# Performance work log

Measured on AMD Instinct MI355X. Metric: run time of the kernel, lower is better.

Reference implementation:

```python
import jax, jax.numpy as jnp
import numpy as np

EMBED_DIM = 1024
NUM_HEADS = 16
HEAD_DIM = EMBED_DIM // NUM_HEADS
MAX_REL = 64
B, S = 4, 1024


def setup_inputs() -> dict:
    key = jax.random.key(0)
    ks = jax.random.split(key, 12)
    scale = 1.0 / np.sqrt(EMBED_DIM)
    inp = {
        "query": jax.random.normal(ks[0], (B, S, EMBED_DIM), jnp.float32),
        "key": jax.random.normal(ks[1], (B, S, EMBED_DIM), jnp.float32),
        "value": jax.random.normal(ks[2], (B, S, EMBED_DIM), jnp.float32),
        "attn_mask": jnp.ones((B, 1, S, S), jnp.int32),
        # projection weights stored [in, out] so x @ W matches torch Linear(x) with W = weight.T
        "Wq": jax.random.normal(ks[3], (EMBED_DIM, EMBED_DIM), jnp.float32) * scale,
        "bq": jnp.zeros((EMBED_DIM,), jnp.float32),
        "Wk": jax.random.normal(ks[4], (EMBED_DIM, EMBED_DIM), jnp.float32) * scale,
        "bk": jnp.zeros((EMBED_DIM,), jnp.float32),
        "Wv": jax.random.normal(ks[5], (EMBED_DIM, EMBED_DIM), jnp.float32) * scale,
        "bv": jnp.zeros((EMBED_DIM,), jnp.float32),
        "Wo": jax.random.normal(ks[6], (EMBED_DIM, EMBED_DIM), jnp.float32) * scale,
        "bo": jnp.zeros((EMBED_DIM,), jnp.float32),
        "rel_pos_embed": jax.random.normal(ks[7], (2 * MAX_REL + 1, HEAD_DIM), jnp.float32) * 0.02,
    }
    return inp


def _split_heads(x):
    # [B, S, E] -> [B, H, S, D]
    b, s, _ = x.shape
    return x.reshape(b, s, NUM_HEADS, HEAD_DIM).transpose(0, 2, 1, 3)


def reference(query, key, value, attn_mask, Wq, bq, Wk, bk, Wv, bv, Wo, bo, rel_pos_embed):
    q = _split_heads(query @ Wq + bq)
    k = _split_heads(key @ Wk + bk)
    v = _split_heads(value @ Wv + bv)

    scores = jnp.einsum("bhqd,bhkd->bhqk", q, k) / np.sqrt(HEAD_DIM).astype(np.float32)

    # relative position bias: rel_pos[i, j] = rel_pos_embed[clip(i - j) + MAX_REL]
    seq_len = scores.shape[-1]
    rng = jnp.arange(seq_len)
    range_mat = jnp.clip(rng[:, None] - rng[None, :], -MAX_REL, MAX_REL) + MAX_REL
    rel_pos = rel_pos_embed[range_mat]                       # [S, S, D]
    # torch: matmul(q[...,None,:], rel_pos.mT).squeeze(-2) == einsum over head_dim (NOT scaled)
    rel_scores = jnp.einsum("bhid,ijd->bhij", q, rel_pos)
    scores = scores + rel_scores

    scores = jnp.where(attn_mask == 0, -jnp.inf, scores)
    attn_weights = jax.nn.softmax(scores, axis=-1)           # dropout p=0.0 -> identity

    out = jnp.einsum("bhqk,bhkd->bhqd", attn_weights, v)
    out = out.transpose(0, 2, 1, 3).reshape(query.shape[0], -1, EMBED_DIM)
    out = out @ Wo + bo
    return out, attn_weights
```

## Files before the change

### kernel.cpp

```cpp
#include <hip/hip_runtime.h>
#include <math.h>

#define BB 4
#define SS 1024
#define EE 1024
#define HH 16
#define DD 64
#define RR 129
#define PRELW 130

typedef __attribute__((ext_vector_type(4))) float f32x4;
typedef __attribute__((ext_vector_type(4))) int   i32x4;
typedef __attribute__((ext_vector_type(8))) short bf8;
typedef __attribute__((ext_vector_type(4))) short s4v;

#define MFMA(a, b, c) __builtin_amdgcn_mfma_f32_16x16x32_bf16(a, b, c, 0, 0, 0)

__device__ __forceinline__ float bf2f(unsigned short u) {
    return __uint_as_float(((unsigned)u) << 16);
}
__device__ __forceinline__ unsigned short f2bf(float x) {
    unsigned u = __float_as_uint(x);
    return (unsigned short)((u + 0x7fffu + ((u >> 16) & 1u)) >> 16);
}

__global__ __launch_bounds__(256, 4)
void wtrans_kernel(const float* __restrict__ Wq, const float* __restrict__ Wk,
                   const float* __restrict__ Wv, const float* __restrict__ Wo,
                   unsigned short* __restrict__ wt_hi, unsigned short* __restrict__ wt_lo)
{
    __shared__ float T[64][65];
    const int w = blockIdx.z;
    const float* W = w == 0 ? Wq : (w == 1 ? Wk : (w == 2 ? Wv : Wo));
    const int n0 = blockIdx.x * 64, k0 = blockIdx.y * 64;
    const int tid = threadIdx.x;
#pragma unroll
    for (int i = 0; i < 4; ++i) {
        int c = tid + 256 * i; int r = c >> 4, c4 = c & 15;
        f32x4 v = *(const f32x4*)(W + (size_t)(k0 + r) * EE + n0 + c4 * 4);
        T[r][c4 * 4 + 0] = v.x; T[r][c4 * 4 + 1] = v.y;
        T[r][c4 * 4 + 2] = v.z; T[r][c4 * 4 + 3] = v.w;
    }
    __syncthreads();
#pragma unroll
    for (int i = 0; i < 4; ++i) {
        int c = tid + 256 * i; int r = c >> 4, c4 = c & 15;
        float x0 = T[c4 * 4 + 0][r], x1 = T[c4 * 4 + 1][r];
        float x2 = T[c4 * 4 + 2][r], x3 = T[c4 * 4 + 3][r];
        unsigned short h0 = f2bf(x0), h1 = f2bf(x1), h2 = f2bf(x2), h3 = f2bf(x3);
        unsigned short l0 = f2bf(x0 - bf2f(h0)), l1 = f2bf(x1 - bf2f(h1));
        unsigned short l2 = f2bf(x2 - bf2f(h2)), l3 = f2bf(x3 - bf2f(h3));
        size_t o = (size_t)w * 1048576 + (size_t)(n0 + r) * 1024 + k0 + c4 * 4;
        *(s4v*)&wt_hi[o] = (s4v){(short)h0, (short)h1, (short)h2, (short)h3};
        *(s4v*)&wt_lo[o] = (s4v){(short)l0, (short)l1, (short)l2, (short)l3};
    }
}

__global__ __launch_bounds__(256)
void maskbits_kernel(const int* __restrict__ mask, unsigned long long* __restrict__ mb)
{
    const int w = blockIdx.x * 256 + threadIdx.x;
    const int* p = mask + (size_t)w * 64;
    unsigned long long bits = 0;
#pragma unroll
    for (int i = 0; i < 16; ++i) {
        int4 v = *(const int4*)(p + i * 4);
        bits |= (unsigned long long)(v.x != 0) << (i * 4 + 0);
        bits |= (unsigned long long)(v.y != 0) << (i * 4 + 1);
        bits |= (unsigned long long)(v.z != 0) << (i * 4 + 2);
        bits |= (unsigned long long)(v.w != 0) << (i * 4 + 3);
    }
    mb[w] = bits;
}

template<int ASRC, int EPI>
__device__ __forceinline__ void gemm_body(
    const float* __restrict__ Af,
    const unsigned short* __restrict__ Ah_g, const unsigned short* __restrict__ Al_g,
    const unsigned short* __restrict__ Bh_g, const unsigned short* __restrict__ Bl_g,
    const float* __restrict__ bias,
    float* __restrict__ Yf, unsigned short* __restrict__ Yh, unsigned short* __restrict__ Yl,
    unsigned short* As_h, unsigned short* As_l, unsigned short* Bs_h, unsigned short* Bs_l,
    int m0, int n0)
{
    const int tid = threadIdx.x, lane = tid & 63, wid = tid >> 6;
    const int wm = (wid >> 1) * 64, wn = (wid & 1) * 64;
    f32x4 zero4 = {0.f, 0.f, 0.f, 0.f};
    f32x4 acc[4][4];
#pragma unroll
    for (int a = 0; a < 4; ++a)
#pragma unroll
        for (int b = 0; b < 4; ++b) acc[a][b] = zero4;

    for (int kt = 0; kt < 1024; kt += 64) {
        __syncthreads();
        if (ASRC == 0) {
#pragma unroll
            for (int i = 0; i < 8; ++i) {
                int c = tid + 256 * i; int r = c >> 4, c4 = c & 15;
                f32x4 v = *(const f32x4*)(Af + (size_t)(m0 + r) * 1024 + kt + c4 * 4);
                unsigned short h0 = f2bf(v.x), h1 = f2bf(v.y), h2 = f2bf(v.z), h3 = f2bf(v.w);
                unsigned short l0 = f2bf(v.x - bf2f(h0)), l1 = f2bf(v.y - bf2f(h1));
                unsigned short l2 = f2bf(v.z - bf2f(h2)), l3 = f2bf(v.w - bf2f(h3));
                int off = r * 64 + (((c4 >> 1) ^ (r & 7)) * 8) + (c4 & 1) * 4;
                *(s4v*)&As_h[off] = (s4v){(short)h0, (short)h1, (short)h2, (short)h3};
                *(s4v*)&As_l[off] = (s4v){(short)l0, (short)l1, (short)l2, (short)l3};
            }
        } else {
#pragma unroll
            for (int i = 0; i < 4; ++i) {
                int c = tid + 256 * i; int r = c >> 3, cc = c & 7;
                int off = r * 64 + ((cc ^ (r & 7)) * 8);
                *(bf8*)&As_h[off] = *(const bf8*)(Ah_g + (size_t)(m0 + r) * 1024 + kt + cc * 8);
                *(bf8*)&As_l[off] = *(const bf8*)(Al_g + (size_t)(m0 + r) * 1024 + kt + cc * 8);
            }
        }
#pragma unroll
        for (int i = 0; i < 4; ++i) {
            int c = tid + 256 * i; int r = c >> 3, cc = c & 7;
            int off = r * 64 + ((cc ^ (r & 7)) * 8);
            *(bf8*)&Bs_h[off] = *(const bf8*)(Bh_g + (size_t)(n0 + r) * 1024 + kt + cc * 8);
            *(bf8*)&Bs_l[off] = *(const bf8*)(Bl_g + (size_t)(n0 + r) * 1024 + kt + cc * 8);
        }
        __syncthreads();
#pragma unroll
        for (int ks = 0; ks < 2; ++ks) {
            bf8 ah[4], al[4], bh[4], bl[4];
#pragma unroll
            for (int f = 0; f < 4; ++f) {
                int ra = wm + f * 16 + (lane & 15);
                int ca = (ks * 4 + (lane >> 4)) ^ (ra & 7);
                ah[f] = *(const bf8*)&As_h[ra * 64 + ca * 8];
                al[f] = *(const bf8*)&As_l[ra * 64 + ca * 8];
                int rb = wn + f * 16 + (lane & 15);
                int cb = (ks * 4 + (lane >> 4)) ^ (rb & 7);
                bh[f] = *(const bf8*)&Bs_h[rb * 64 + cb * 8];
                bl[f] = *(const bf8*)&Bs_l[rb * 64 + cb * 8];
            }
#pragma unroll
            for (int fi = 0; fi < 4; ++fi)
#pragma unroll
                for (int fj = 0; fj < 4; ++fj) {
                    acc[fi][fj] = MFMA(ah[fi], bh[fj], acc[fi][fj]);
                    acc[fi][fj] = MFMA(al[fi], bh[fj], acc[fi][fj]);
                    acc[fi][fj] = MFMA(ah[fi], bl[fj], acc[fi][fj]);
                }
        }
    }
#pragma unroll
    for (int fi = 0; fi < 4; ++fi)
#pragma unroll
        for (int fj = 0; fj < 4; ++fj)
#pragma unroll
            for (int rg = 0; rg < 4; ++rg) {
                int m = m0 + wm + fi * 16 + ((lane >> 4) << 2) + rg;
                int n = n0 + wn + fj * 16 + (lane & 15);
                float val = acc[fi][fj][rg] + bias[n];
                if (EPI == 0) {
                    int b = m >> 10, s = m & 1023, h = n >> 6, d = n & 63;
                    size_t o = (((size_t)(b * 16 + h)) * 1024 + s) * 64 + d;
                    unsigned short hv = f2bf(val);
                    unsigned short lv = f2bf(val - bf2f(hv));
                    Yh[o] = hv; Yl[o] = lv;
                } else {
                    Yf[(size_t)m * 1024 + n] = val;
                }
            }
}

__global__ __launch_bounds__(256, 2)
void proj_qkv_kernel(const float* __restrict__ q_in, const float* __restrict__ k_in,
                     const float* __restrict__ v_in,
                     const unsigned short* __restrict__ wt_hi, const unsigned short* __restrict__ wt_lo,
                     const float* __restrict__ bq, const float* __restrict__ bk,
                     const float* __restrict__ bv,
                     unsigned short* qh_hi, unsigned short* qh_lo,
                     unsigned short* kh_hi, unsigned short* kh_lo,
                     unsigned short* vh_hi, unsigned short* vh_lo)
{
    __shared__ __align__(16) unsigned short As_h[128 * 64], As_l[128 * 64];
    __shared__ __align__(16) unsigned short Bs_h[128 * 64], Bs_l[128 * 64];
    const int z = blockIdx.z;
    const float* X = z == 0 ? q_in : (z == 1 ? k_in : v_in);
    const float* bias = z == 0 ? bq : (z == 1 ? bk : bv);
    unsigned short* Yh = z == 0 ? qh_hi : (z == 1 ? kh_hi : vh_hi);
    unsigned short* Yl = z == 0 ? qh_lo : (z == 1 ? kh_lo : vh_lo);
    gemm_body<0, 0>(X, nullptr, nullptr,
                    wt_hi + (size_t)z * 1048576, wt_lo + (size_t)z * 1048576,
                    bias, nullptr, Yh, Yl, As_h, As_l, Bs_h, Bs_l,
                    blockIdx.x * 128, blockIdx.y * 128);
}

__global__ __launch_bounds__(256, 2)
void outproj_kernel(const unsigned short* __restrict__ ctx_hi, const unsigned short* __restrict__ ctx_lo,
                    const unsigned short* __restrict__ wo_hi, const unsigned short* __restrict__ wo_lo,
                    const float* __restrict__ bo, float* __restrict__ out)
{
    __shared__ __align__(16) unsigned short As_h[128 * 64], As_l[128 * 64];
    __shared__ __align__(16) unsigned short Bs_h[128 * 64], Bs_l[128 * 64];
    gemm_body<1, 1>(nullptr, ctx_hi, ctx_lo, wo_hi, wo_lo, bo, out, nullptr, nullptr,
                    As_h, As_l, Bs_h, Bs_l, blockIdx.x * 128, blockIdx.y * 128);
}

__global__ __launch_bounds__(256, 4)
void vtrans_kernel(const unsigned short* __restrict__ vh_hi, const unsigned short* __restrict__ vh_lo,
                   unsigned short* __restrict__ vt_hi, unsigned short* __restrict__ vt_lo)
{
    __shared__ unsigned short T[64][72];
    const unsigned short* src = blockIdx.z ? vh_lo : vh_hi;
    unsigned short* dst = blockIdx.z ? vt_lo : vt_hi;
    const int st = blockIdx.x * 64, bh = blockIdx.y, tid = threadIdx.x;
#pragma unroll
    for (int i = 0; i < 4; ++i) {
        int c = tid + 256 * i; int r = c >> 4, d4 = c & 15;
        s4v v = *(const s4v*)(src + ((size_t)bh * 1024 + st + r) * 64 + d4 * 4);
        T[r][d4 * 4 + 0] = (unsigned short)v.x; T[r][d4 * 4 + 1] = (unsigned short)v.y;
        T[r][d4 * 4 + 2] = (unsigned short)v.z; T[r][d4 * 4 + 3] = (unsigned short)v.w;
    }
    __syncthreads();
#pragma unroll
    for (int i = 0; i < 4; ++i) {
        int c = tid + 256 * i; int r = c >> 4, s4_ = c & 15;
        s4v o = {(short)T[s4_ * 4 + 0][r], (short)T[s4_ * 4 + 1][r],
                 (short)T[s4_ * 4 + 2][r], (short)T[s4_ * 4 + 3][r]};
        *(s4v*)(dst + ((size_t)bh * 64 + r) * 1024 + st + s4_ * 4) = o;
    }
}

__global__ __launch_bounds__(256, 2)
void attn_fused_kernel(const unsigned short* __restrict__ qh_hi, const unsigned short* __restrict__ qh_lo,
                       const unsigned short* __restrict__ kh_hi, const unsigned short* __restrict__ kh_lo,
                       const unsigned short* __restrict__ vt_hi, const unsigned short* __restrict__ vt_lo,
                       const float* __restrict__ emb, const unsigned long long* __restrict__ mb,
                       float* __restrict__ attn,
                       unsigned short* __restrict__ ctx_hi, unsigned short* __restrict__ ctx_lo)
{
    __shared__ __align__(16) unsigned short Sh[128 * 64], Sl[128 * 64];
    __shared__ __align__(16) unsigned short Pr[128 * PRELW];
    __shared__ float Sm[2][128], Ss[2][128], SmF[128], SsF[128];
    const int tid = threadIdx.x, lane = tid & 63, wid = tid >> 6;
    const int wi = wid >> 1, wj = wid & 1;
    const int g = lane >> 4, li = lane & 15;
    const int bh = blockIdx.x, i0 = blockIdx.y * 128, b = bh >> 4;
    const f32x4 zero4 = {0.f, 0.f, 0.f, 0.f};

    const unsigned short* qbh = qh_hi + ((size_t)bh * 1024 + i0) * 64;
    const unsigned short* qbl = qh_lo + ((size_t)bh * 1024 + i0) * 64;
#pragma unroll
    for (int i = 0; i < 4; ++i) {
        int c = tid + 256 * i; int r = c >> 3, cc = c & 7;
        int off = r * 64 + ((cc ^ (r & 7)) * 8);
        *(bf8*)&Sh[off] = *(const bf8*)(qbh + r * 64 + cc * 8);
        *(bf8*)&Sl[off] = *(const bf8*)(qbl + r * 64 + cc * 8);
    }
    __syncthreads();

    bf8 qfh[4][2], qfl[4][2];
#pragma unroll
    for (int fi = 0; fi < 4; ++fi)
#pragma unroll
        for (int ks = 0; ks < 2; ++ks) {
            int rb = wi * 64 + fi * 16 + li;
            int cb = (ks * 4 + g) ^ (rb & 7);
            qfh[fi][ks] = *(const bf8*)&Sh[rb * 64 + cb * 8];
            qfl[fi][ks] = *(const bf8*)&Sl[rb * 64 + cb * 8];
        }

    for (int t = wid; t < 72; t += 4) {
        const int it = t / 9, rt = t % 9;
        f32x4 pc = zero4;
#pragma unroll
        for (int ks = 0; ks < 2; ++ks) {
            int ra = it * 16 + li;
            int ca = (ks * 4 + g) ^ (ra & 7);
            bf8 aq = *(const bf8*)&Sh[ra * 64 + ca * 8];
            int er = rt * 16 + li; if (er > 128) er = 128;
            const float* ep = emb + (size_t)er * 64 + ks * 32 + g * 8;
            f32x4 e0 = *(const f32x4*)ep;
            f32x4 e1 = *(const f32x4*)(ep + 4);
            bf8 be = {(short)f2bf(e0.x), (short)f2bf(e0.y), (short)f2bf(e0.z), (short)f2bf(e0.w),
                      (short)f2bf(e1.x), (short)f2bf(e1.y), (short)f2bf(e1.z), (short)f2bf(e1.w)};
            pc = MFMA(aq, be, pc);
        }
        const int rcol = rt * 16 + li;
        if (rcol < RR) {
#pragma unroll
            for (int rg = 0; rg < 4; ++rg)
                Pr[(it * 16 + g * 4 + rg) * PRELW + rcol] = f2bf(pc[rg]);
        }
    }

    float rm[4], rs[4];
#pragma unroll
    for (int i = 0; i < 4; ++i) { rm[i] = -3.0e38f; rs[i] = 0.f; }

    for (int jt = 0; jt < 8; ++jt) {
        __syncthreads();
        const unsigned short* kbh = kh_hi + ((size_t)bh * 1024 + jt * 128) * 64;
        const unsigned short* kbl = kh_lo + ((size_t)bh * 1024 + jt * 128) * 64;
#pragma unroll
        for (int i = 0; i < 4; ++i) {
            int c = tid + 256 * i; int r = c >> 3, cc = c & 7;
            int off = r * 64 + ((cc ^ (r & 7)) * 8);
            *(bf8*)&Sh[off] = *(const bf8*)(kbh + r * 64 + cc * 8);
            *(bf8*)&Sl[off] = *(const bf8*)(kbl + r * 64 + cc * 8);
        }
        __syncthreads();
        f32x4 acc[4][4];
#pragma unroll
        for (int a = 0; a < 4; ++a)
#pragma unroll
            for (int c = 0; c < 4; ++c) acc[a][c] = zero4;
#pragma unroll
        for (int ks = 0; ks < 2; ++ks) {
            bf8 kfh[4], kfl[4];
#pragma unroll
            for (int fj = 0; fj < 4; ++fj) {
                int ra = wj * 64 + fj * 16 + li;
                int ca = (ks * 4 + g) ^ (ra & 7);
                kfh[fj] = *(const bf8*)&Sh[ra * 64 + ca * 8];
                kfl[fj] = *(const bf8*)&Sl[ra * 64 + ca * 8];
            }
#pragma unroll
            for (int fj = 0; fj < 4; ++fj)
#pragma unroll
                for (int fi = 0; fi < 4; ++fi) {
                    acc[fj][fi] = MFMA(kfh[fj], qfh[fi][ks], acc[fj][fi]);
                    acc[fj][fi] = MFMA(kfl[fj], qfh[fi][ks], acc[fj][fi]);
                    acc[fj][fi] = MFMA(kfh[fj], qfl[fi][ks], acc[fj][fi]);
                }
        }
#pragma unroll
        for (int fi = 0; fi < 4; ++fi) {
            const int rowL = wi * 64 + fi * 16 + li;
            const int ii = i0 + rowL;
            const unsigned long long mw = mb[((size_t)b * 1024 + ii) * 16 + jt * 2 + wj];
            float p16[4][4];
            float tmax = -3.0e38f;
#pragma unroll
            for (int fj = 0; fj < 4; ++fj)
#pragma unroll
                for (int rg = 0; rg < 4; ++rg) {
                    int jloc = fj * 16 + g * 4 + rg;
                    int jj = jt * 128 + wj * 64 + jloc;
                    int dd = ii - jj; dd = dd < -64 ? -64 : (dd > 64 ? 64 : dd);
                    float s = acc[fj][fi][rg] * 0.125f + bf2f(Pr[rowL * PRELW + dd + 64]);
                    if (!((mw >> jloc) & 1ull)) s = -1.0e30f;
                    p16[fj][rg] = s;
                    tmax = fmaxf(tmax, s);
                }
            tmax = fmaxf(tmax, __shfl_xor(tmax, 16, 64));
            tmax = fmaxf(tmax, __shfl_xor(tmax, 32, 64));
            float nm = fmaxf(rm[fi], tmax);
            float ps = 0.f;
#pragma unroll
            for (int fj = 0; fj < 4; ++fj)
#pragma unroll
                for (int rg = 0; rg < 4; ++rg) ps += __expf(p16[fj][rg] - nm);
            ps += __shfl_xor(ps, 16, 64);
            ps += __shfl_xor(ps, 32, 64);
            rs[fi] = rs[fi] * __expf(rm[fi] - nm) + ps;
            rm[fi] = nm;
        }
    }
#pragma unroll
    for (int fi = 0; fi < 4; ++fi) {
        if (lane < 16) {
            Sm[wj][wi * 64 + fi * 16 + li] = rm[fi];
            Ss[wj][wi * 64 + fi * 16 + li] = rs[fi];
        }
    }
    __syncthreads();
    if (tid < 128) {
        float m0_ = Sm[0][tid], m1_ = Sm[1][tid];
        float mmx = fmaxf(m0_, m1_);
        SmF[tid] = mmx;
        SsF[tid] = Ss[0][tid] * __expf(m0_ - mmx) + Ss[1][tid] * __expf(m1_ - mmx);
    }
    __syncthreads();
    float mm4[4], iv4[4];
#pragma unroll
    for (int fi = 0; fi < 4; ++fi) {
        mm4[fi] = SmF[wi * 64 + fi * 16 + li];
        iv4[fi] = 1.f / SsF[wi * 64 + fi * 16 + li];
    }

    f32x4 ctx_acc[4][4];
#pragma unroll
    for (int a = 0; a < 4; ++a)
#pragma unroll
        for (int c = 0; c < 4; ++c) ctx_acc[a][c] = zero4;

    for (int jt = 0; jt < 8; ++jt) {
        __syncthreads();
        const unsigned short* kbh = kh_hi + ((size_t)bh * 1024 + jt * 128) * 64;
        const unsigned short* kbl = kh_lo + ((size_t)bh * 1024 + jt * 128) * 64;
#pragma unroll
        for (int i = 0; i < 4; ++i) {
            int c = tid + 256 * i; int r = c >> 3, cc = c & 7;
            int off = r * 64 + ((cc ^ (r & 7)) * 8);
            *(bf8*)&Sh[off] = *(const bf8*)(kbh + r * 64 + cc * 8);
            *(bf8*)&Sl[off] = *(const bf8*)(kbl + r * 64 + cc * 8);
        }
        __syncthreads();
        f32x4 acc[4][4];
#pragma unroll
        for (int a = 0; a < 4; ++a)
#pragma unroll
            for (int c = 0; c < 4; ++c) acc[a][c] = zero4;
#pragma unroll
        for (int ks = 0; ks < 2; ++ks) {
            bf8 kfh[4], kfl[4];
#pragma unroll
            for (int fj = 0; fj < 4; ++fj) {
                int ra = wj * 64 + fj * 16 + li;
                int ca = (ks * 4 + g) ^ (ra & 7);
                kfh[fj] = *(const bf8*)&Sh[ra * 64 + ca * 8];
                kfl[fj] = *(const bf8*)&Sl[ra * 64 + ca * 8];
            }
#pragma unroll
            for (int fj = 0; fj < 4; ++fj)
#pragma unroll
                for (int fi = 0; fi < 4; ++fi) {
                    acc[fj][fi] = MFMA(kfh[fj], qfh[fi][ks], acc[fj][fi]);
                    acc[fj][fi] = MFMA(kfl[fj], qfh[fi][ks], acc[fj][fi]);
                    acc[fj][fi] = MFMA(kfh[fj], qfl[fi][ks], acc[fj][fi]);
                }
        }
#pragma unroll
        for (int c = 0; c < 2; ++c) {
            bf8 vfh[4], vfl[4];
#pragma unroll
            for (int fd = 0; fd < 4; ++fd) {
                size_t vb = (size_t)bh * 65536 + (size_t)(fd * 16 + li) * 1024
                          + jt * 128 + wj * 64 + c * 32 + g * 8;
                vfh[fd] = *(const bf8*)(vt_hi + vb);
                vfl[fd] = *(const bf8*)(vt_lo + vb);
            }
#pragma unroll
            for (int fi = 0; fi < 4; ++fi) {
                const int rowL = wi * 64 + fi * 16 + li;
                const int ii = i0 + rowL;
                const unsigned long long mw = mb[((size_t)b * 1024 + ii) * 16 + jt * 2 + wj];
                const float mmf = mm4[fi], ivf = iv4[fi];
                float* arow = attn + ((size_t)bh * 1024 + ii) * 1024 + jt * 128 + wj * 64 + g * 4;
                unsigned wh[2][2], wl[2][2];
#pragma unroll
                for (int t = 0; t < 2; ++t) {
                    const int fj = c * 2 + t;
                    f32x4 pv;
#pragma unroll
                    for (int rg = 0; rg < 4; ++rg) {
                        int jloc = fj * 16 + g * 4 + rg;
                        int jj = jt * 128 + wj * 64 + jloc;
                        int dd = ii - jj; dd = dd < -64 ? -64 : (dd > 64 ? 64 : dd);
                        float s = acc[fj][fi][rg] * 0.125f + bf2f(Pr[rowL * PRELW + dd + 64]);
                        if (!((mw >> jloc) & 1ull)) s = -1.0e30f;
                        pv[rg] = __expf(s - mmf) * ivf;
                    }
                    *(f32x4*)(arow + fj * 16) = pv;
                    unsigned short h0 = f2bf(pv.x), h1 = f2bf(pv.y), h2 = f2bf(pv.z), h3 = f2bf(pv.w);
                    wh[t][0] = (unsigned)h0 | ((unsigned)h1 << 16);
                    wh[t][1] = (unsigned)h2 | ((unsigned)h3 << 16);
                    unsigned short l0 = f2bf(pv.x - bf2f(h0)), l1 = f2bf(pv.y - bf2f(h1));
                    unsigned short l2 = f2bf(pv.z - bf2f(h2)), l3 = f2bf(pv.w - bf2f(h3));
                    wl[t][0] = (unsigned)l0 | ((unsigned)l1 << 16);
                    wl[t][1] = (unsigned)l2 | ((unsigned)l3 << 16);
                }
                const int src0 = ((g & 1) * 2) * 16 + li;
                const int src1 = src0 + 16;
                const bool hiT = (g >> 1) & 1;
                int x0A = __shfl((int)wh[0][0], src0, 64), x0B = __shfl((int)wh[1][0], src0, 64);
                int x1A = __shfl((int)wh[0][1], src0, 64), x1B = __shfl((int)wh[1][1], src0, 64);
                int x2A = __shfl((int)wh[0][0], src1, 64), x2B = __shfl((int)wh[1][0], src1, 64);
                int x3A = __shfl((int)wh[0][1], src1, 64), x3B = __shfl((int)wh[1][1], src1, 64);
                i32x4 awh = {hiT ? x0B : x0A, hiT ? x1B : x1A, hiT ? x2B : x2A, hiT ? x3B : x3A};
                bf8 pah = *(bf8*)&awh;
                int y0A = __shfl((int)wl[0][0], src0, 64), y0B = __shfl((int)wl[1][0], src0, 64);
                int y1A = __shfl((int)wl[0][1], src0, 64), y1B = __shfl((int)wl[1][1], src0, 64);
                int y2A = __shfl((int)wl[0][0], src1, 64), y2B = __shfl((int)wl[1][0], src1, 64);
                int y3A = __shfl((int)wl[0][1], src1, 64), y3B = __shfl((int)wl[1][1], src1, 64);
                i32x4 awl = {hiT ? y0B : y0A, hiT ? y1B : y1A, hiT ? y2B : y2A, hiT ? y3B : y3A};
                bf8 pal = *(bf8*)&awl;
#pragma unroll
                for (int fd = 0; fd < 4; ++fd) {
                    ctx_acc[fi][fd] = MFMA(pah, vfh[fd], ctx_acc[fi][fd]);
                    ctx_acc[fi][fd] = MFMA(pal, vfh[fd], ctx_acc[fi][fd]);
                    ctx_acc[fi][fd] = MFMA(pah, vfl[fd], ctx_acc[fi][fd]);
                }
            }
        }
    }

    __syncthreads();
    float* red = (wi == 0) ? (float*)Sh : (float*)Sl;
    if (wj == 1) {
#pragma unroll
        for (int fi = 0; fi < 4; ++fi)
#pragma unroll
            for (int fd = 0; fd < 4; ++fd)
#pragma unroll
                for (int rg = 0; rg < 4; ++rg) {
                    int idx = (fi * 4 + fd) * 4 + rg;
                    red[lane * 64 + ((idx + lane) & 63)] = ctx_acc[fi][fd][rg];
                }
    }
    __syncthreads();
    if (wj == 0) {
        const int b_ = bh >> 4, h = bh & 15;
#pragma unroll
        for (int fi = 0; fi < 4; ++fi)
#pragma unroll
            for (int fd = 0; fd < 4; ++fd)
#pragma unroll
                for (int rg = 0; rg < 4; ++rg) {
                    int idx = (fi * 4 + fd) * 4 + rg;
                    float val = ctx_acc[fi][fd][rg] + red[lane * 64 + ((idx + lane) & 63)];
                    int ii = i0 + wi * 64 + fi * 16 + g * 4 + rg;
                    int d = fd * 16 + li;
                    size_t o = ((size_t)b_ * 1024 + ii) * 1024 + h * 64 + d;
                    unsigned short hv = f2bf(val);
                    unsigned short lv = f2bf(val - bf2f(hv));
                    ctx_hi[o] = hv;
                    ctx_lo[o] = lv;
                }
    }
}

extern "C" void kernel_launch(void* const* d_in, const int* in_sizes, int n_in,
                              void* d_out, int out_size, void* d_ws, size_t ws_size,
                              hipStream_t stream)
{
    const float* query = (const float*)d_in[0];
    const float* key_  = (const float*)d_in[1];
    const float* value = (const float*)d_in[2];
    const int*   mask  = (const int*)d_in[3];
    const float* Wq = (const float*)d_in[4];
    const float* bq = (const float*)d_in[5];
    const float* Wk = (const float*)d_in[6];
    const float* bk = (const float*)d_in[7];
    const float* Wv = (const float*)d_in[8];
    const float* bv = (const float*)d_in[9];
    const float* Wo = (const float*)d_in[10];
    const float* bo = (const float*)d_in[11];
    const float* emb = (const float*)d_in[12];

    unsigned short* wt_hi = (unsigned short*)d_ws;
    unsigned short* wt_lo = wt_hi + (size_t)4 * 1048576;
    unsigned short* qh_hi = wt_lo + (size_t)4 * 1048576;
    unsigned short* qh_lo = qh_hi + 4194304;
    unsigned short* kh_hi = qh_lo + 4194304;
    unsigned short* kh_lo = kh_hi + 4194304;
    unsigned short* vt_hi = kh_lo + 4194304;
    unsigned short* vt_lo = vt_hi + 4194304;
    unsigned short* ctx_hi = vt_lo + 4194304;
    unsigned short* ctx_lo = ctx_hi + 4194304;
    unsigned long long* mb = (unsigned long long*)d_ws;
    unsigned short* vh_hi = (unsigned short*)d_out;
    unsigned short* vh_lo = vh_hi + 4194304;

    float* out  = (float*)d_out;
    float* attn = (float*)d_out + 4194304;

    dim3 blk(256);
    wtrans_kernel<<<dim3(16, 16, 4), blk, 0, stream>>>(Wq, Wk, Wv, Wo, wt_hi, wt_lo);
    proj_qkv_kernel<<<dim3(32, 8, 3), blk, 0, stream>>>(query, key_, value, wt_hi, wt_lo,
                                                        bq, bk, bv, qh_hi, qh_lo,
                                                        kh_hi, kh_lo, vh_hi, vh_lo);
    maskbits_kernel<<<dim3(256), blk, 0, stream>>>(mask, mb);
    vtrans_kernel<<<dim3(16, 64, 2), blk, 0, stream>>>(vh_hi, vh_lo, vt_hi, vt_lo);
    attn_fused_kernel<<<dim3(64, 8), blk, 0, stream>>>(qh_hi, qh_lo, kh_hi, kh_lo,
                                                       vt_hi, vt_lo, emb, mb,
                                                       attn, ctx_hi, ctx_lo);
    outproj_kernel<<<dim3(32, 8), blk, 0, stream>>>(ctx_hi, ctx_lo,
                                                    wt_hi + (size_t)3 * 1048576,
                                                    wt_lo + (size_t)3 * 1048576, bo, out);
}
```

Before: 539.2 us.

## Halve K tile to 64 rows to cut LDS and registers for three blocks per CU

Shrinks the shared K/Q staging buffers from 128 to 64 rows, loads Q and builds the relative-position table in two 64-row halves, and iterates the key loop 16 times with 64-key tiles. This lowers per-thread accumulator registers and LDS usage so launch bounds can request three blocks per CU, aiming at more latency hiding. The final cross-wave reduction buffer moves into the Pr region, and attention-weight stores become nontemporal to avoid polluting cache. The cost is twice as many barriers and tile loads, and smaller MFMA batches per sync.

```diff
diff --git a/kernel.cpp b/kernel.cpp
--- a/kernel.cpp
+++ b/kernel.cpp
@@ -227,7 +227,7 @@
     }
 }
 
-__global__ __launch_bounds__(256, 2)
+__global__ __launch_bounds__(256, 3)
 void attn_fused_kernel(const unsigned short* __restrict__ qh_hi, const unsigned short* __restrict__ qh_lo,
                        const unsigned short* __restrict__ kh_hi, const unsigned short* __restrict__ kh_lo,
                        const unsigned short* __restrict__ vt_hi, const unsigned short* __restrict__ vt_lo,
@@ -235,7 +235,7 @@
                        float* __restrict__ attn,
                        unsigned short* __restrict__ ctx_hi, unsigned short* __restrict__ ctx_lo)
 {
-    __shared__ __align__(16) unsigned short Sh[128 * 64], Sl[128 * 64];
+    __shared__ __align__(16) unsigned short Sh[64 * 64], Sl[64 * 64];
     __shared__ __align__(16) unsigned short Pr[128 * PRELW];
     __shared__ float Sm[2][128], Ss[2][128], SmF[128], SsF[128];
     const int tid = threadIdx.x, lane = tid & 63, wid = tid >> 6;
@@ -246,83 +246,87 @@
 
     const unsigned short* qbh = qh_hi + ((size_t)bh * 1024 + i0) * 64;
     const unsigned short* qbl = qh_lo + ((size_t)bh * 1024 + i0) * 64;
-#pragma unroll
-    for (int i = 0; i < 4; ++i) {
-        int c = tid + 256 * i; int r = c >> 3, cc = c & 7;
-        int off = r * 64 + ((cc ^ (r & 7)) * 8);
-        *(bf8*)&Sh[off] = *(const bf8*)(qbh + r * 64 + cc * 8);
-        *(bf8*)&Sl[off] = *(const bf8*)(qbl + r * 64 + cc * 8);
-    }
-    __syncthreads();
 
     bf8 qfh[4][2], qfl[4][2];
 #pragma unroll
-    for (int fi = 0; fi < 4; ++fi)
-#pragma unroll
-        for (int ks = 0; ks < 2; ++ks) {
-            int rb = wi * 64 + fi * 16 + li;
-            int cb = (ks * 4 + g) ^ (rb & 7);
-            qfh[fi][ks] = *(const bf8*)&Sh[rb * 64 + cb * 8];
-            qfl[fi][ks] = *(const bf8*)&Sl[rb * 64 + cb * 8];
-        }
-
-    for (int t = wid; t < 72; t += 4) {
-        const int it = t / 9, rt = t % 9;
-        f32x4 pc = zero4;
-#pragma unroll
-        for (int ks = 0; ks < 2; ++ks) {
-            int ra = it * 16 + li;
-            int ca = (ks * 4 + g) ^ (ra & 7);
-            bf8 aq = *(const bf8*)&Sh[ra * 64 + ca * 8];
-            int er = rt * 16 + li; if (er > 128) er = 128;
-            const float* ep = emb + (size_t)er * 64 + ks * 32 + g * 8;
-            f32x4 e0 = *(const f32x4*)ep;
-            f32x4 e1 = *(const f32x4*)(ep + 4);
-            bf8 be = {(short)f2bf(e0.x), (short)f2bf(e0.y), (short)f2bf(e0.z), (short)f2bf(e0.w),
-                      (short)f2bf(e1.x), (short)f2bf(e1.y), (short)f2bf(e1.z), (short)f2bf(e1.w)};
-            pc = MFMA(aq, be, pc);
-        }
-        const int rcol = rt * 16 + li;
-        if (rcol < RR) {
-#pragma unroll
-            for (int rg = 0; rg < 4; ++rg)
-                Pr[(it * 16 + g * 4 + rg) * PRELW + rcol] = f2bf(pc[rg]);
-        }
+    for (int h = 0; h < 2; ++h) {
+#pragma unroll
+        for (int i = 0; i < 2; ++i) {
+            int c = tid + 256 * i; int r = c >> 3, cc = c & 7;
+            int off = r * 64 + ((cc ^ (r & 7)) * 8);
+            *(bf8*)&Sh[off] = *(const bf8*)(qbh + (size_t)(h * 64 + r) * 64 + cc * 8);
+            *(bf8*)&Sl[off] = *(const bf8*)(qbl + (size_t)(h * 64 + r) * 64 + cc * 8);
+        }
+        __syncthreads();
+        if (wi == h) {
+#pragma unroll
+            for (int fi = 0; fi < 4; ++fi)
+#pragma unroll
+                for (int ks = 0; ks < 2; ++ks) {
+                    int rb = fi * 16 + li;
+                    int cb = (ks * 4 + g) ^ (rb & 7);
+                    qfh[fi][ks] = *(const bf8*)&Sh[rb * 64 + cb * 8];
+                    qfl[fi][ks] = *(const bf8*)&Sl[rb * 64 + cb * 8];
+                }
+        }
+        for (int t = wid; t < 36; t += 4) {
+            const int itl = t / 9, rt = t % 9;
+            f32x4 pc = zero4;
+#pragma unroll
+            for (int ks = 0; ks < 2; ++ks) {
+                int ra = itl * 16 + li;
+                int ca = (ks * 4 + g) ^ (ra & 7);
+                bf8 aq = *(const bf8*)&Sh[ra * 64 + ca * 8];
+                int er = rt * 16 + li; if (er > 128) er = 128;
+                const float* ep = emb + (size_t)er * 64 + ks * 32 + g * 8;
+                f32x4 e0 = *(const f32x4*)ep;
+                f32x4 e1 = *(const f32x4*)(ep + 4);
+                bf8 be = {(short)f2bf(e0.x), (short)f2bf(e0.y), (short)f2bf(e0.z), (short)f2bf(e0.w),
+                          (short)f2bf(e1.x), (short)f2bf(e1.y), (short)f2bf(e1.z), (short)f2bf(e1.w)};
+                pc = MFMA(aq, be, pc);
+            }
+            const int rcol = rt * 16 + li;
+            if (rcol < RR) {
+#pragma unroll
+                for (int rg = 0; rg < 4; ++rg)
+                    Pr[(h * 64 + itl * 16 + g * 4 + rg) * PRELW + rcol] = f2bf(pc[rg]);
+            }
+        }
+        __syncthreads();
     }
 
     float rm[4], rs[4];
 #pragma unroll
     for (int i = 0; i < 4; ++i) { rm[i] = -3.0e38f; rs[i] = 0.f; }
 
-    for (int jt = 0; jt < 8; ++jt) {
-        __syncthreads();
-        const unsigned short* kbh = kh_hi + ((size_t)bh * 1024 + jt * 128) * 64;
-        const unsigned short* kbl = kh_lo + ((size_t)bh * 1024 + jt * 128) * 64;
-#pragma unroll
-        for (int i = 0; i < 4; ++i) {
+    for (int jt = 0; jt < 16; ++jt) {
+        const unsigned short* kbh = kh_hi + ((size_t)bh * 1024 + jt * 64) * 64;
+        const unsigned short* kbl = kh_lo + ((size_t)bh * 1024 + jt * 64) * 64;
+#pragma unroll
+        for (int i = 0; i < 2; ++i) {
             int c = tid + 256 * i; int r = c >> 3, cc = c & 7;
             int off = r * 64 + ((cc ^ (r & 7)) * 8);
             *(bf8*)&Sh[off] = *(const bf8*)(kbh + r * 64 + cc * 8);
             *(bf8*)&Sl[off] = *(const bf8*)(kbl + r * 64 + cc * 8);
         }
         __syncthreads();
-        f32x4 acc[4][4];
-#pragma unroll
-        for (int a = 0; a < 4; ++a)
+        f32x4 acc[2][4];
+#pragma unroll
+        for (int a = 0; a < 2; ++a)
 #pragma unroll
             for (int c = 0; c < 4; ++c) acc[a][c] = zero4;
 #pragma unroll
         for (int ks = 0; ks < 2; ++ks) {
-            bf8 kfh[4], kfl[4];
-#pragma unroll
-            for (int fj = 0; fj < 4; ++fj) {
-                int ra = wj * 64 + fj * 16 + li;
+            bf8 kfh[2], kfl[2];
+#pragma unroll
+            for (int fj = 0; fj < 2; ++fj) {
+                int ra = wj * 32 + fj * 16 + li;
                 int ca = (ks * 4 + g) ^ (ra & 7);
                 kfh[fj] = *(const bf8*)&Sh[ra * 64 + ca * 8];
                 kfl[fj] = *(const bf8*)&Sl[ra * 64 + ca * 8];
             }
 #pragma unroll
-            for (int fj = 0; fj < 4; ++fj)
+            for (int fj = 0; fj < 2; ++fj)
 #pragma unroll
                 for (int fi = 0; fi < 4; ++fi) {
                     acc[fj][fi] = MFMA(kfh[fj], qfh[fi][ks], acc[fj][fi]);
@@ -334,18 +338,18 @@
         for (int fi = 0; fi < 4; ++fi) {
             const int rowL = wi * 64 + fi * 16 + li;
             const int ii = i0 + rowL;
-            const unsigned long long mw = mb[((size_t)b * 1024 + ii) * 16 + jt * 2 + wj];
-            float p16[4][4];
+            const unsigned long long mw = mb[((size_t)b * 1024 + ii) * 16 + jt];
+            float p16[2][4];
             float tmax = -3.0e38f;
 #pragma unroll
-            for (int fj = 0; fj < 4; ++fj)
+            for (int fj = 0; fj < 2; ++fj)
 #pragma unroll
                 for (int rg = 0; rg < 4; ++rg) {
                     int jloc = fj * 16 + g * 4 + rg;
-                    int jj = jt * 128 + wj * 64 + jloc;
+                    int jj = jt * 64 + wj * 32 + jloc;
                     int dd = ii - jj; dd = dd < -64 ? -64 : (dd > 64 ? 64 : dd);
                     float s = acc[fj][fi][rg] * 0.125f + bf2f(Pr[rowL * PRELW + dd + 64]);
-                    if (!((mw >> jloc) & 1ull)) s = -1.0e30f;
+                    if (!((mw >> (wj * 32 + jloc)) & 1ull)) s = -1.0e30f;
                     p16[fj][rg] = s;
                     tmax = fmaxf(tmax, s);
                 }
@@ -354,7 +358,7 @@
             float nm = fmaxf(rm[fi], tmax);
             float ps = 0.f;
 #pragma unroll
-            for (int fj = 0; fj < 4; ++fj)
+            for (int fj = 0; fj < 2; ++fj)
 #pragma unroll
                 for (int rg = 0; rg < 4; ++rg) ps += __expf(p16[fj][rg] - nm);
             ps += __shfl_xor(ps, 16, 64);
@@ -362,6 +366,7 @@
             rs[fi] = rs[fi] * __expf(rm[fi] - nm) + ps;
             rm[fi] = nm;
         }
+        __syncthreads();
     }
 #pragma unroll
     for (int fi = 0; fi < 4; ++fi) {
@@ -391,35 +396,34 @@
 #pragma unroll
         for (int c = 0; c < 4; ++c) ctx_acc[a][c] = zero4;
 
-    for (int jt = 0; jt < 8; ++jt) {
-        __syncthreads();
-        const unsigned short* kbh = kh_hi + ((size_t)bh * 1024 + jt * 128) * 64;
-        const unsigned short* kbl = kh_lo + ((size_t)bh * 1024 + jt * 128) * 64;
-#pragma unroll
-        for (int i = 0; i < 4; ++i) {
+    for (int jt = 0; jt < 16; ++jt) {
+        const unsigned short* kbh = kh_hi + ((size_t)bh * 1024 + jt * 64) * 64;
+        const unsigned short* kbl = kh_lo + ((size_t)bh * 1024 + jt * 64) * 64;
+#pragma unroll
+        for (int i = 0; i < 2; ++i) {
             int c = tid + 256 * i; int r = c >> 3, cc = c & 7;
             int off = r * 64 + ((cc ^ (r & 7)) * 8);
             *(bf8*)&Sh[off] = *(const bf8*)(kbh + r * 64 + cc * 8);
             *(bf8*)&Sl[off] = *(const bf8*)(kbl + r * 64 + cc * 8);
         }
         __syncthreads();
-        f32x4 acc[4][4];
-#pragma unroll
-        for (int a = 0; a < 4; ++a)
+        f32x4 acc[2][4];
+#pragma unroll
+        for (int a = 0; a < 2; ++a)
 #pragma unroll
             for (int c = 0; c < 4; ++c) acc[a][c] = zero4;
 #pragma unroll
         for (int ks = 0; ks < 2; ++ks) {
-            bf8 kfh[4], kfl[4];
-#pragma unroll
-            for (int fj = 0; fj < 4; ++fj) {
-                int ra = wj * 64 + fj * 16 + li;
+            bf8 kfh[2], kfl[2];
+#pragma unroll
+            for (int fj = 0; fj < 2; ++fj) {
+                int ra = wj * 32 + fj * 16 + li;
                 int ca = (ks * 4 + g) ^ (ra & 7);
                 kfh[fj] = *(const bf8*)&Sh[ra * 64 + ca * 8];
                 kfl[fj] = *(const bf8*)&Sl[ra * 64 + ca * 8];
             }
 #pragma unroll
-            for (int fj = 0; fj < 4; ++fj)
+            for (int fj = 0; fj < 2; ++fj)
 #pragma unroll
                 for (int fi = 0; fi < 4; ++fi) {
                     acc[fj][fi] = MFMA(kfh[fj], qfh[fi][ks], acc[fj][fi]);
@@ -427,73 +431,70 @@
                     acc[fj][fi] = MFMA(kfh[fj], qfl[fi][ks], acc[fj][fi]);
                 }
         }
-#pragma unroll
-        for (int c = 0; c < 2; ++c) {
-            bf8 vfh[4], vfl[4];
+        bf8 vfh[4], vfl[4];
+#pragma unroll
+        for (int fd = 0; fd < 4; ++fd) {
+            size_t vb = (size_t)bh * 65536 + (size_t)(fd * 16 + li) * 1024
+                      + jt * 64 + wj * 32 + g * 8;
+            vfh[fd] = *(const bf8*)(vt_hi + vb);
+            vfl[fd] = *(const bf8*)(vt_lo + vb);
+        }
+#pragma unroll
+        for (int fi = 0; fi < 4; ++fi) {
+            const int rowL = wi * 64 + fi * 16 + li;
+            const int ii = i0 + rowL;
+            const unsigned long long mw = mb[((size_t)b * 1024 + ii) * 16 + jt];
+            const float mmf = mm4[fi], ivf = iv4[fi];
+            float* arow = attn + ((size_t)bh * 1024 + ii) * 1024 + jt * 64 + wj * 32 + g * 4;
+            unsigned wh[2][2], wl[2][2];
+#pragma unroll
+            for (int t = 0; t < 2; ++t) {
+                const int fj = t;
+                f32x4 pv;
+#pragma unroll
+                for (int rg = 0; rg < 4; ++rg) {
+                    int jloc = fj * 16 + g * 4 + rg;
+                    int jj = jt * 64 + wj * 32 + jloc;
+                    int dd = ii - jj; dd = dd < -64 ? -64 : (dd > 64 ? 64 : dd);
+                    float s = acc[fj][fi][rg] * 0.125f + bf2f(Pr[rowL * PRELW + dd + 64]);
+                    if (!((mw >> (wj * 32 + jloc)) & 1ull)) s = -1.0e30f;
+                    pv[rg] = __expf(s - mmf) * ivf;
+                }
+                __builtin_nontemporal_store(pv, (f32x4*)(arow + t * 16));
+                unsigned short h0 = f2bf(pv.x), h1 = f2bf(pv.y), h2 = f2bf(pv.z), h3 = f2bf(pv.w);
+                wh[t][0] = (unsigned)h0 | ((unsigned)h1 << 16);
+                wh[t][1] = (unsigned)h2 | ((unsigned)h3 << 16);
+                unsigned short l0 = f2bf(pv.x - bf2f(h0)), l1 = f2bf(pv.y - bf2f(h1));
+                unsigned short l2 = f2bf(pv.z - bf2f(h2)), l3 = f2bf(pv.w - bf2f(h3));
+                wl[t][0] = (unsigned)l0 | ((unsigned)l1 << 16);
+                wl[t][1] = (unsigned)l2 | ((unsigned)l3 << 16);
+            }
+            const int src0 = ((g & 1) * 2) * 16 + li;
+            const int src1 = src0 + 16;
+            const bool hiT = (g >> 1) & 1;
+            int x0A = __shfl((int)wh[0][0], src0, 64), x0B = __shfl((int)wh[1][0], src0, 64);
+            int x1A = __shfl((int)wh[0][1], src0, 64), x1B = __shfl((int)wh[1][1], src0, 64);
+            int x2A = __shfl((int)wh[0][0], src1, 64), x2B = __shfl((int)wh[1][0], src1, 64);
+            int x3A = __shfl((int)wh[0][1], src1, 64), x3B = __shfl((int)wh[1][1], src1, 64);
+            i32x4 awh = {hiT ? x0B : x0A, hiT ? x1B : x1A, hiT ? x2B : x2A, hiT ? x3B : x3A};
+            bf8 pah = *(bf8*)&awh;
+            int y0A = __shfl((int)wl[0][0], src0, 64), y0B = __shfl((int)wl[1][0], src0, 64);
+            int y1A = __shfl((int)wl[0][1], src0, 64), y1B = __shfl((int)wl[1][1], src0, 64);
+            int y2A = __shfl((int)wl[0][0], src1, 64), y2B = __shfl((int)wl[1][0], src1, 64);
+            int y3A = __shfl((int)wl[0][1], src1, 64), y3B = __shfl((int)wl[1][1], src1, 64);
+            i32x4 awl = {hiT ? y0B : y0A, hiT ? y1B : y1A, hiT ? y2B : y2A, hiT ? y3B : y3A};
+            bf8 pal = *(bf8*)&awl;
 #pragma unroll
             for (int fd = 0; fd < 4; ++fd) {
-                size_t vb = (size_t)bh * 65536 + (size_t)(fd * 16 + li) * 1024
-                          + jt * 128 + wj * 64 + c * 32 + g * 8;
-                vfh[fd] = *(const bf8*)(vt_hi + vb);
-                vfl[fd] = *(const bf8*)(vt_lo + vb);
-            }
-#pragma unroll
-            for (int fi = 0; fi < 4; ++fi) {
-                const int rowL = wi * 64 + fi * 16 + li;
-                const int ii = i0 + rowL;
-                const unsigned long long mw = mb[((size_t)b * 1024 + ii) * 16 + jt * 2 + wj];
-                const float mmf = mm4[fi], ivf = iv4[fi];
-                float* arow = attn + ((size_t)bh * 1024 + ii) * 1024 + jt * 128 + wj * 64 + g * 4;
-                unsigned wh[2][2], wl[2][2];
-#pragma unroll
-                for (int t = 0; t < 2; ++t) {
-                    const int fj = c * 2 + t;
-                    f32x4 pv;
-#pragma unroll
-                    for (int rg = 0; rg < 4; ++rg) {
-                        int jloc = fj * 16 + g * 4 + rg;
-                        int jj = jt * 128 + wj * 64 + jloc;
-                        int dd = ii - jj; dd = dd < -64 ? -64 : (dd > 64 ? 64 : dd);
-                        float s = acc[fj][fi][rg] * 0.125f + bf2f(Pr[rowL * PRELW + dd + 64]);
-                        if (!((mw >> jloc) & 1ull)) s = -1.0e30f;
-                        pv[rg] = __expf(s - mmf) * ivf;
-                    }
-                    *(f32x4*)(arow + fj * 16) = pv;
-                    unsigned short h0 = f2bf(pv.x), h1 = f2bf(pv.y), h2 = f2bf(pv.z), h3 = f2bf(pv.w);
-                    wh[t][0] = (unsigned)h0 | ((unsigned)h1 << 16);
-                    wh[t][1] = (unsigned)h2 | ((unsigned)h3 << 16);
-                    unsigned short l0 = f2bf(pv.x - bf2f(h0)), l1 = f2bf(pv.y - bf2f(h1));
-                    unsigned short l2 = f2bf(pv.z - bf2f(h2)), l3 = f2bf(pv.w - bf2f(h3));
-                    wl[t][0] = (unsigned)l0 | ((unsigned)l1 << 16);
-                    wl[t][1] = (unsigned)l2 | ((unsigned)l3 << 16);
-                }
-                const int src0 = ((g & 1) * 2) * 16 + li;
-                const int src1 = src0 + 16;
-                const bool hiT = (g >> 1) & 1;
-                int x0A = __shfl((int)wh[0][0], src0, 64), x0B = __shfl((int)wh[1][0], src0, 64);
-                int x1A = __shfl((int)wh[0][1], src0, 64), x1B = __shfl((int)wh[1][1], src0, 64);
-                int x2A = __shfl((int)wh[0][0], src1, 64), x2B = __shfl((int)wh[1][0], src1, 64);
-                int x3A = __shfl((int)wh[0][1], src1, 64), x3B = __shfl((int)wh[1][1], src1, 64);
-                i32x4 awh = {hiT ? x0B : x0A, hiT ? x1B : x1A, hiT ? x2B : x2A, hiT ? x3B : x3A};
-                bf8 pah = *(bf8*)&awh;
-                int y0A = __shfl((int)wl[0][0], src0, 64), y0B = __shfl((int)wl[1][0], src0, 64);
-                int y1A = __shfl((int)wl[0][1], src0, 64), y1B = __shfl((int)wl[1][1], src0, 64);
-                int y2A = __shfl((int)wl[0][0], src1, 64), y2B = __shfl((int)wl[1][0], src1, 64);
-                int y3A = __shfl((int)wl[0][1], src1, 64), y3B = __shfl((int)wl[1][1], src1, 64);
-                i32x4 awl = {hiT ? y0B : y0A, hiT ? y1B : y1A, hiT ? y2B : y2A, hiT ? y3B : y3A};
-                bf8 pal = *(bf8*)&awl;
-#pragma unroll
-                for (int fd = 0; fd < 4; ++fd) {
-                    ctx_acc[fi][fd] = MFMA(pah, vfh[fd], ctx_acc[fi][fd]);
-                    ctx_acc[fi][fd] = MFMA(pal, vfh[fd], ctx_acc[fi][fd]);
-                    ctx_acc[fi][fd] = MFMA(pah, vfl[fd], ctx_acc[fi][fd]);
-                }
-            }
-        }
-    }
-
-    __syncthreads();
-    float* red = (wi == 0) ? (float*)Sh : (float*)Sl;
+                ctx_acc[fi][fd] = MFMA(pah, vfh[fd], ctx_acc[fi][fd]);
+                ctx_acc[fi][fd] = MFMA(pal, vfh[fd], ctx_acc[fi][fd]);
+                ctx_acc[fi][fd] = MFMA(pah, vfl[fd], ctx_acc[fi][fd]);
+            }
+        }
+        __syncthreads();
+    }
+
+    float* red = (float*)Pr + (size_t)wi * 4096;
     if (wj == 1) {
 #pragma unroll
         for (int fi = 0; fi < 4; ++fi)
```

After: 581.2 us. 7.8% more time.
